# Performance work log

Hardware: AMD Instinct MI355X
Metric: run time of the kernel (lower is better)

Reference implementation:

```python
import jax, jax.numpy as jnp
import numpy as np

EPS = 1e-4  # matches normalize()/pixel_norm eps in the torch source
MP_T = 0.3  # mp_add mixing coefficient


def _weight_norm_1x1(w):
    # w: [out, in, 1, 1]; normalize each output filter (dims 1..3), alpha = 1/sqrt(fan_in),
    # then divide by sqrt(fan_in) as in Conv2d.forward (eval mode: no in-place copy).
    fan_in = w.shape[1] * w.shape[2] * w.shape[3]
    inv_sqrt_fan = np.float32(1.0 / np.sqrt(fan_in))
    n = jnp.sqrt(jnp.sum(w * w, axis=(1, 2, 3), keepdims=True))
    w_hat = w / (EPS + inv_sqrt_fan * n)
    return w_hat * inv_sqrt_fan


def _conv1x1(x, w):
    # 1x1 conv == channel GEMM
    return jnp.einsum('oc,bchw->bohw', _weight_norm_1x1(w)[:, :, 0, 0], x)


def _pixel_norm_last(x):
    # x / sqrt(mean(x^2, axis=-1) + eps)
    ms = jnp.mean(x * x, axis=-1, keepdims=True)
    return x * jax.lax.rsqrt(ms + EPS)


def setup_inputs() -> dict:
    key = jax.random.key(0)
    k1, k2, k3 = jax.random.split(key, 3)
    x = jax.random.normal(k1, (2, 256, 64, 64), dtype=jnp.float32)
    w_qkv = jax.random.normal(k2, (768, 256, 1, 1), dtype=jnp.float32)
    w_out = jax.random.normal(k3, (256, 256, 1, 1), dtype=jnp.float32)
    return {"x": x, "w_qkv": w_qkv, "w_out": w_out, "num_heads": 8}


def reference(x, w_qkv, w_out, num_heads):
    b, c, h, w = x.shape
    head_dim = c // num_heads
    qkv = _conv1x1(x, w_qkv)                      # [b, 3c, h, w]
    q, k, v = jnp.split(qkv, 3, axis=1)           # each [b, c, h, w]

    def to_heads(t):
        # [b, c, h, w] -> [b, heads, hw, head_dim]
        return t.reshape(b, num_heads, head_dim, h * w).transpose(0, 1, 3, 2)

    q = _pixel_norm_last(to_heads(q))
    k = _pixel_norm_last(to_heads(k))
    v = _pixel_norm_last(to_heads(v))

    scale = np.float32(1.0 / np.sqrt(head_dim))
    scores = jnp.einsum('bhqd,bhkd->bhqk', q, k) * scale
    attn = jax.nn.softmax(scores, axis=-1)
    y = jnp.einsum('bhqk,bhkd->bhqd', attn, v)    # [b, heads, hw, head_dim]
    y = y.transpose(0, 1, 3, 2).reshape(b, c, h, w)
    y = _conv1x1(y, w_out)

    # mp_add(x, y, t=0.3)
    t = np.float32(MP_T)
    inv_scale = np.float32(1.0 / np.sqrt(MP_T ** 2 + (1.0 - MP_T) ** 2))
    return ((1.0 - t) * x + t * y) * inv_scale
```

## Files before the change

kernel.cpp:

```cpp
#include <hip/hip_runtime.h>
#include <hip/hip_bf16.h>
#include <math.h>

#define S 4096
#define CIN 256
#define C3 768
#define NH 8
#define HD 32
#define KSPLIT 4

static constexpr float EPS = 1e-4f;

typedef __attribute__((ext_vector_type(8))) __bf16 bf16x8;
typedef __attribute__((ext_vector_type(4))) float f32x4;
typedef __attribute__((ext_vector_type(16))) float f32x16;
typedef __attribute__((ext_vector_type(4))) unsigned u32x4;

static inline __device__ ushort f2bf(float f) {
  unsigned u = __float_as_uint(f);
  return (ushort)((u + 0x7fffu + ((u >> 16) & 1u)) >> 16);
}
static inline __device__ float bf2f(ushort u) {
  return __uint_as_float((unsigned)u << 16);
}

static inline __device__ unsigned cvt_pk_bf16(float lo, float hi) {
  unsigned r;
  asm("v_cvt_pk_bf16_f32 %0, %1, %2" : "=v"(r) : "v"(lo), "v"(hi));
  return r;
}
static inline __device__ void plane32_swap(unsigned& a, unsigned& b) {
  asm("v_permlane32_swap_b32 %0, %1" : "+v"(a), "+v"(b));
}

#define EXP2 __builtin_amdgcn_exp2f


static inline __device__ void s_to_pf(const f32x16 s, bf16x8& plo, bf16x8& phi,
                                      float& lacc) {
  float e0 = EXP2(s[0]), e1 = EXP2(s[1]), e2 = EXP2(s[2]), e3 = EXP2(s[3]);
  float e4 = EXP2(s[4]), e5 = EXP2(s[5]), e6 = EXP2(s[6]), e7 = EXP2(s[7]);
  float e8 = EXP2(s[8]), e9 = EXP2(s[9]), e10 = EXP2(s[10]), e11 = EXP2(s[11]);
  float e12 = EXP2(s[12]), e13 = EXP2(s[13]), e14 = EXP2(s[14]), e15 = EXP2(s[15]);
  lacc += (((e0 + e1) + (e2 + e3)) + ((e4 + e5) + (e6 + e7))) +
          (((e8 + e9) + (e10 + e11)) + ((e12 + e13) + (e14 + e15)));
  unsigned c0 = cvt_pk_bf16(e0, e1);
  unsigned c1 = cvt_pk_bf16(e2, e3);
  unsigned c2 = cvt_pk_bf16(e4, e5);
  unsigned c3 = cvt_pk_bf16(e6, e7);
  plane32_swap(c0, c2);
  plane32_swap(c1, c3);
  u32x4 lo4 = {c0, c1, c2, c3};
  plo = __builtin_bit_cast(bf16x8, lo4);
  unsigned c4 = cvt_pk_bf16(e8, e9);
  unsigned c5 = cvt_pk_bf16(e10, e11);
  unsigned c6 = cvt_pk_bf16(e12, e13);
  unsigned c7 = cvt_pk_bf16(e14, e15);
  plane32_swap(c4, c6);
  plane32_swap(c5, c7);
  u32x4 hi4 = {c4, c5, c6, c7};
  phi = __builtin_bit_cast(bf16x8, hi4);
}

__global__ __launch_bounds__(256) void wnorm_kernel(const float* __restrict__ w_qkv,
                                                    const float* __restrict__ w_out,
                                                    ushort* __restrict__ wqb,
                                                    ushort* __restrict__ wob) {
  const int row = blockIdx.x * 4 + (threadIdx.x >> 6);
  const int lane = threadIdx.x & 63;
  const bool is_q = row < C3;
  const int r2 = is_q ? row : row - C3;
  const float* wr = (is_q ? w_qkv : w_out) + (size_t)r2 * CIN;
  float v[4];
  #pragma unroll
  for (int i = 0; i < 4; i++) v[i] = wr[lane + 64 * i];
  float ss = v[0] * v[0] + v[1] * v[1] + v[2] * v[2] + v[3] * v[3];
  #pragma unroll
  for (int off = 32; off > 0; off >>= 1) ss += __shfl_down(ss, off, 64);
  ss = __shfl(ss, 0, 64);
  const float scale = 1.0f / (sqrtf(ss) + 16.0f * EPS);
  ushort* whr = (is_q ? wqb : wob);
  #pragma unroll
  for (int i = 0; i < 4; i++) {
    const int c = lane + 64 * i;
    whr[((size_t)(r2 >> 4) * (CIN / 32) + (c >> 5)) * 512 + (r2 & 15) * 32 + (c & 31)] =
        f2bf(v[i] * scale);
  }
}

__global__ __launch_bounds__(256) void xt_kernel(const float* __restrict__ X,
                                                 ushort* __restrict__ Xt) {
  const int b = blockIdx.z;
  const int s0 = blockIdx.x * 64, c0 = blockIdx.y * 64;
  __shared__ ushort T[64][72];
  const int tc = threadIdx.x >> 4;
  const int ts = threadIdx.x & 15;
  #pragma unroll
  for (int i = 0; i < 4; i++) {
    const float4 v = *(const float4*)&X[((size_t)(b * CIN + c0 + tc + 16 * i)) * S + s0 + ts * 4];
    ushort4 u;
    u.x = f2bf(v.x); u.y = f2bf(v.y); u.z = f2bf(v.z); u.w = f2bf(v.w);
    *(ushort4*)&T[tc + 16 * i][ts * 4] = u;
  }
  __syncthreads();
  #pragma unroll
  for (int i = 0; i < 4; i++) {
    const int sr = tc + 16 * i;
    const int s = s0 + sr;
    const int c = c0 + ts * 4;
    ushort4 u;
    u.x = T[ts * 4 + 0][sr];
    u.y = T[ts * 4 + 1][sr];
    u.z = T[ts * 4 + 2][sr];
    u.w = T[ts * 4 + 3][sr];
    *(ushort4*)&Xt[(((size_t)b * (S / 16) + (s >> 4)) * (CIN / 32) + (c >> 5)) * 512 +
                   (s & 15) * 32 + (c & 31)] = u;
  }
}

__global__ __launch_bounds__(256) void conv1_fused_kernel(const ushort* __restrict__ W,
                                                          const ushort* __restrict__ Bm,
                                                          ushort* __restrict__ Qn,
                                                          ushort* __restrict__ Kn,
                                                          ushort* __restrict__ Vt) {
  const int b = blockIdx.z;
  const int wid = threadIdx.x >> 6, lane = threadIdx.x & 63;
  const int col = lane & 15, quad = lane >> 4;
  const int m0 = blockIdx.y * 64 + (wid >> 1) * 32;
  const int n0 = blockIdx.x * 128 + (wid & 1) * 64;
  const ushort* Bb = Bm + (size_t)b * (S / 16) * (CIN / 32) * 512;
  const int lofs = col * 32 + quad * 8;
  f32x4 acc[2][4] = {};
  #pragma unroll
  for (int k0 = 0; k0 < CIN; k0 += 32) {
    bf16x8 af[2], bf[4];
    #pragma unroll
    for (int mi = 0; mi < 2; mi++)
      af[mi] = *(const bf16x8*)&W[((size_t)(m0 / 16 + mi) * (CIN / 32) + (k0 >> 5)) * 512 + lofs];
    #pragma unroll
    for (int ni = 0; ni < 4; ni++)
      bf[ni] = *(const bf16x8*)&Bb[((size_t)(n0 / 16 + ni) * (CIN / 32) + (k0 >> 5)) * 512 + lofs];
    #pragma unroll
    for (int mi = 0; mi < 2; mi++)
      #pragma unroll
      for (int ni = 0; ni < 4; ni++)
        acc[mi][ni] = __builtin_amdgcn_mfma_f32_16x16x32_bf16(af[mi], bf[ni], acc[mi][ni], 0, 0, 0);
  }

  const int g = m0 >> 5;
  const int h = g & 7;
  float rn[4];
  #pragma unroll
  for (int ni = 0; ni < 4; ni++) {
    float ss = 0.f;
    #pragma unroll
    for (int mi = 0; mi < 2; mi++)
      #pragma unroll
      for (int r = 0; r < 4; r++) ss += acc[mi][ni][r] * acc[mi][ni][r];
    ss += __shfl_xor(ss, 16, 64);
    ss += __shfl_xor(ss, 32, 64);
    rn[ni] = rsqrtf(ss * (1.0f / HD) + EPS);
    if (g < 8) rn[ni] *= 0.2550348190698169f;
  }

  if (g < 8) {
    ushort* dst = Qn + (size_t)(b * NH + h) * S * HD;
    #pragma unroll
    for (int mi = 0; mi < 2; mi++)
      #pragma unroll
      for (int ni = 0; ni < 4; ni++) {
        ushort4 u;
        u.x = f2bf(acc[mi][ni][0] * rn[ni]);
        u.y = f2bf(acc[mi][ni][1] * rn[ni]);
        u.z = f2bf(acc[mi][ni][2] * rn[ni]);
        u.w = f2bf(acc[mi][ni][3] * rn[ni]);
        *(ushort4*)&dst[(size_t)(n0 + ni * 16 + col) * HD + mi * 16 + quad * 4] = u;
      }
  } else if (g < 16) {
    ushort* dst = Kn + (size_t)(b * NH + h) * S * HD + (size_t)(n0 >> 5) * 1024;
    #pragma unroll
    for (int mi = 0; mi < 2; mi++)
      #pragma unroll
      for (int ni = 0; ni < 4; ni++) {
        ushort4 u;
        u.x = f2bf(acc[mi][ni][0] * rn[ni]);
        u.y = f2bf(acc[mi][ni][1] * rn[ni]);
        u.z = f2bf(acc[mi][ni][2] * rn[ni]);
        u.w = f2bf(acc[mi][ni][3] * rn[ni]);
        *(ushort4*)&dst[(ni >> 1) * 1024 + mi * 512 + ((ni & 1) * 16 + col) * 16 +
                        (quad >> 1) * 8 + (quad & 1) * 4] = u;
      }
  } else {
    ushort* dst = Vt + (size_t)(b * NH + h) * HD * S + (size_t)(n0 >> 6) * 2048;
    #pragma unroll
    for (int mi = 0; mi < 2; mi++)
      #pragma unroll
      for (int ni = 0; ni < 4; ni++)
        #pragma unroll
        for (int r = 0; r < 4; r++)
          dst[ni * 512 + (mi * 16 + quad * 4 + r) * 16 + col] =
              f2bf(acc[mi][ni][r] * rn[ni]);
  }
}

__global__ __launch_bounds__(256, 4) void attn_kernel(const ushort* __restrict__ Qn,
                                                      const ushort* __restrict__ Kn,
                                                      const ushort* __restrict__ Vt,
                                                      ushort* __restrict__ accPb,
                                                      float* __restrict__ lP) {
  const int NWG = (S / 256) * NH * KSPLIT * 2;
  const int bid = blockIdx.x;
  const int id = (bid & 7) * (NWG / 8) + (bid >> 3);
  const int qt = id & 15;
  const int grp = id >> 4;
  const int h = grp & 7;
  const int kp = (grp >> 3) & (KSPLIT - 1);
  const int b = (grp >> 3) / KSPLIT;
  const int wid = threadIdx.x >> 6, lane = threadIdx.x & 63;
  const int ln = lane & 31, hi = lane >> 5;
  const int qA = qt * 256 + wid * 64;
  const int qB = qA + 32;

  const ushort* Qh = Qn + (size_t)(b * NH + h) * S * HD;

  bf16x8 qfA0 = *(const bf16x8*)&Qh[(size_t)(qA + ln) * HD + hi * 8];
  bf16x8 qfA1 = *(const bf16x8*)&Qh[(size_t)(qA + ln) * HD + 16 + hi * 8];
  bf16x8 qfB0 = *(const bf16x8*)&Qh[(size_t)(qB + ln) * HD + hi * 8];
  bf16x8 qfB1 = *(const bf16x8*)&Qh[(size_t)(qB + ln) * HD + 16 + hi * 8];

  const f32x16 z = {};
  f32x16 accA = {}, accB = {};
  float laccA = 0.f, laccB = 0.f;

  const int kt0 = kp * (S / KSPLIT);
  const int loff = (ln * 2 + hi) * 8;
  const ushort* Kp = Kn + (size_t)(b * NH + h) * S * HD + (size_t)kt0 * 32 + loff;
  const ushort* Vp = Vt + (size_t)(b * NH + h) * HD * S + (size_t)kt0 * 32 + loff;

  bf16x8 kf0 = *(const bf16x8*)&Kp[0];
  bf16x8 kf1 = *(const bf16x8*)&Kp[512];
  bf16x8 vf0 = *(const bf16x8*)&Vp[0];
  bf16x8 vf1 = *(const bf16x8*)&Vp[512];

  #pragma unroll 1
  for (int it = 0; it < S / KSPLIT / 32; ++it) {
    f32x16 sA = __builtin_amdgcn_mfma_f32_32x32x16_bf16(kf0, qfA0, z, 0, 0, 0);
    sA = __builtin_amdgcn_mfma_f32_32x32x16_bf16(kf1, qfA1, sA, 0, 0, 0);
    f32x16 sB = __builtin_amdgcn_mfma_f32_32x32x16_bf16(kf0, qfB0, z, 0, 0, 0);
    sB = __builtin_amdgcn_mfma_f32_32x32x16_bf16(kf1, qfB1, sB, 0, 0, 0);
    Kp += 1024;
    kf0 = *(const bf16x8*)&Kp[0];
    kf1 = *(const bf16x8*)&Kp[512];

    bf16x8 pfA0, pfA1;
    s_to_pf(sA, pfA0, pfA1, laccA);
    accA = __builtin_amdgcn_mfma_f32_32x32x16_bf16(vf0, pfA0, accA, 0, 0, 0);
    accA = __builtin_amdgcn_mfma_f32_32x32x16_bf16(vf1, pfA1, accA, 0, 0, 0);

    bf16x8 pfB0, pfB1;
    s_to_pf(sB, pfB0, pfB1, laccB);
    accB = __builtin_amdgcn_mfma_f32_32x32x16_bf16(vf0, pfB0, accB, 0, 0, 0);
    accB = __builtin_amdgcn_mfma_f32_32x32x16_bf16(vf1, pfB1, accB, 0, 0, 0);

    Vp += 1024;
    vf0 = *(const bf16x8*)&Vp[0];
    vf1 = *(const bf16x8*)&Vp[512];
  }

  ushort* ap = accPb + ((size_t)((kp * 2 + b) * NH + h)) * S * HD;
  const size_t rowA = (size_t)(qA + ln) * HD;
  const size_t rowB = (size_t)(qB + ln) * HD;
  #pragma unroll
  for (int g = 0; g < 4; g++) {
    uint2 u;
    u.x = cvt_pk_bf16(accA[4 * g + 0], accA[4 * g + 1]);
    u.y = cvt_pk_bf16(accA[4 * g + 2], accA[4 * g + 3]);
    *(uint2*)&ap[rowA + g * 8 + hi * 4] = u;
    uint2 v;
    v.x = cvt_pk_bf16(accB[4 * g + 0], accB[4 * g + 1]);
    v.y = cvt_pk_bf16(accB[4 * g + 2], accB[4 * g + 3]);
    *(uint2*)&ap[rowB + g * 8 + hi * 4] = v;
  }
  const float lsA = laccA + __shfl_xor(laccA, 32, 64);
  const float lsB = laccB + __shfl_xor(laccB, 32, 64);
  if (hi == 0) {
    float* lp = lP + ((size_t)((kp * 2 + b) * NH + h)) * S;
    lp[qA + ln] = lsA;
    lp[qB + ln] = lsB;
  }
}

__global__ __launch_bounds__(256) void combine_kernel(const ushort* __restrict__ accPb,
                                                      const float* __restrict__ lP,
                                                      ushort* __restrict__ Yt) {
  const int tid = blockIdx.x * 256 + threadIdx.x;
  const int dg = tid & 7;
  const int q = (tid >> 3) & (S - 1);
  const int h = (tid >> 15) & 7;
  const int b = tid >> 18;
  const size_t i0 = ((size_t)(b * NH + h)) * S + q;
  const size_t part = (size_t)2 * NH * S;
  float sx = 0.f, sy = 0.f, sz = 0.f, sw = 0.f, L = 0.f;
  #pragma unroll
  for (int p = 0; p < KSPLIT; p++) {
    const ushort4 a = *(const ushort4*)&accPb[(size_t)p * part * HD + i0 * HD + dg * 4];
    sx += bf2f(a.x); sy += bf2f(a.y); sz += bf2f(a.z); sw += bf2f(a.w);
    L += lP[(size_t)p * part + i0];
  }
  const float rl = 1.0f / L;
  ushort4 o;
  o.x = f2bf(sx * rl);
  o.y = f2bf(sy * rl);
  o.z = f2bf(sz * rl);
  o.w = f2bf(sw * rl);
  *(ushort4*)&Yt[(((size_t)b * (S / 16) + (q >> 4)) * (CIN / 32) + h) * 512 +
                 (q & 15) * 32 + dg * 4] = o;
}

__global__ __launch_bounds__(256) void conv2_kernel(const ushort* __restrict__ W,
                                                    const ushort* __restrict__ Bm,
                                                    const float* __restrict__ RES,
                                                    float* __restrict__ OUT) {
  const int b = blockIdx.z;
  const int wid = threadIdx.x >> 6, lane = threadIdx.x & 63;
  const int col = lane & 15, quad = lane >> 4;
  const int m0 = blockIdx.y * 64 + (wid >> 1) * 32;
  const int n0 = blockIdx.x * 64 + (wid & 1) * 32;
  const ushort* Bb = Bm + (size_t)b * (S / 16) * (CIN / 32) * 512;
  const int lofs = col * 32 + quad * 8;
  f32x4 acc[2][2] = {};
  #pragma unroll
  for (int k0 = 0; k0 < CIN; k0 += 32) {
    bf16x8 af[2], bf[2];
    #pragma unroll
    for (int mi = 0; mi < 2; mi++)
      af[mi] = *(const bf16x8*)&W[((size_t)(m0 / 16 + mi) * (CIN / 32) + (k0 >> 5)) * 512 + lofs];
    #pragma unroll
    for (int ni = 0; ni < 2; ni++)
      bf[ni] = *(const bf16x8*)&Bb[((size_t)(n0 / 16 + ni) * (CIN / 32) + (k0 >> 5)) * 512 + lofs];
    #pragma unroll
    for (int mi = 0; mi < 2; mi++)
      #pragma unroll
      for (int ni = 0; ni < 2; ni++)
        acc[mi][ni] = __builtin_amdgcn_mfma_f32_16x16x32_bf16(af[mi], bf[ni], acc[mi][ni], 0, 0, 0);
  }
  const float tc = 0.3f, om = 0.7f, inv = 1.3130643285972254f;
  #pragma unroll
  for (int mi = 0; mi < 2; mi++)
    #pragma unroll
    for (int ni = 0; ni < 2; ni++)
      #pragma unroll
      for (int r = 0; r < 4; r++) {
        const size_t idx = ((size_t)(b * CIN + m0 + mi * 16 + quad * 4 + r)) * S + n0 + ni * 16 + col;
        OUT[idx] = (om * RES[idx] + tc * acc[mi][ni][r]) * inv;
      }
}

extern "C" void kernel_launch(void* const* d_in, const int* in_sizes, int n_in,
                              void* d_out, int out_size, void* d_ws, size_t ws_size,
                              hipStream_t stream) {
  const float* x = (const float*)d_in[0];
  const float* w_qkv = (const float*)d_in[1];
  const float* w_out = (const float*)d_in[2];
  float* out = (float*)d_out;

  ushort* p = (ushort*)d_ws;
  ushort* wqb = p; p += (size_t)C3 * CIN;
  ushort* wob = p; p += (size_t)CIN * CIN;
  ushort* Qn = p; p += (size_t)2 * NH * S * HD;
  ushort* Kn = p; p += (size_t)2 * NH * S * HD;
  ushort* Vt = p; p += (size_t)2 * NH * S * HD;
  ushort* Yt = p; p += (size_t)2 * S * CIN;
  ushort* R = p; p += (size_t)KSPLIT * 2 * NH * S * HD;
  ushort* Xt = R;
  ushort* accPb = R;
  float* lP = (float*)p;

  wnorm_kernel<<<(C3 + CIN) / 4, 256, 0, stream>>>(w_qkv, w_out, wqb, wob);
  xt_kernel<<<dim3(S / 64, CIN / 64, 2), 256, 0, stream>>>(x, Xt);
  conv1_fused_kernel<<<dim3(S / 128, C3 / 64, 2), 256, 0, stream>>>(wqb, Xt, Qn, Kn, Vt);
  attn_kernel<<<(S / 256) * NH * KSPLIT * 2, 256, 0, stream>>>(Qn, Kn, Vt, accPb, lP);
  combine_kernel<<<2048, 256, 0, stream>>>(accPb, lP, Yt);
  conv2_kernel<<<dim3(S / 64, CIN / 64, 2), 256, 0, stream>>>(wob, Yt, x, out);
}
```

Before: 144.6 us.

## Compute softmax row sums via MFMA with ones and shrink conv1 N tile

The attention loop no longer sums the exponentials with VALU adds. It issues extra MFMAs that multiply the bf16 probabilities by a ones matrix, so the row sums come out of the matrix cores. This shifts work off the VALU, which is busy with exp2 and conversions, at the cost of doubling the PV-stage MFMA count, two extra 16-float accumulators per wave, and row sums taken from bf16-rounded probabilities. Separately, the conv1 kernel's per-wave N tile shrinks from 64 to 32 columns, doubling the grid to raise occupancy, with the K and V store indexing adjusted to match.

```diff
diff --git a/kernel.cpp b/kernel.cpp
--- a/kernel.cpp
+++ b/kernel.cpp
@@ -14,6 +14,7 @@
 typedef __attribute__((ext_vector_type(8))) __bf16 bf16x8;
 typedef __attribute__((ext_vector_type(4))) float f32x4;
 typedef __attribute__((ext_vector_type(16))) float f32x16;
+typedef __attribute__((ext_vector_type(8))) unsigned short u16x8;
 typedef __attribute__((ext_vector_type(4))) unsigned u32x4;
 
 static inline __device__ ushort f2bf(float f) {
@@ -36,26 +37,19 @@
 #define EXP2 __builtin_amdgcn_exp2f
 
 
-static inline __device__ void s_to_pf(const f32x16 s, bf16x8& plo, bf16x8& phi,
-                                      float& lacc) {
-  float e0 = EXP2(s[0]), e1 = EXP2(s[1]), e2 = EXP2(s[2]), e3 = EXP2(s[3]);
-  float e4 = EXP2(s[4]), e5 = EXP2(s[5]), e6 = EXP2(s[6]), e7 = EXP2(s[7]);
-  float e8 = EXP2(s[8]), e9 = EXP2(s[9]), e10 = EXP2(s[10]), e11 = EXP2(s[11]);
-  float e12 = EXP2(s[12]), e13 = EXP2(s[13]), e14 = EXP2(s[14]), e15 = EXP2(s[15]);
-  lacc += (((e0 + e1) + (e2 + e3)) + ((e4 + e5) + (e6 + e7))) +
-          (((e8 + e9) + (e10 + e11)) + ((e12 + e13) + (e14 + e15)));
-  unsigned c0 = cvt_pk_bf16(e0, e1);
-  unsigned c1 = cvt_pk_bf16(e2, e3);
-  unsigned c2 = cvt_pk_bf16(e4, e5);
-  unsigned c3 = cvt_pk_bf16(e6, e7);
+static inline __device__ void s_to_pf(const f32x16 s, bf16x8& plo, bf16x8& phi) {
+  unsigned c0 = cvt_pk_bf16(EXP2(s[0]), EXP2(s[1]));
+  unsigned c1 = cvt_pk_bf16(EXP2(s[2]), EXP2(s[3]));
+  unsigned c2 = cvt_pk_bf16(EXP2(s[4]), EXP2(s[5]));
+  unsigned c3 = cvt_pk_bf16(EXP2(s[6]), EXP2(s[7]));
   plane32_swap(c0, c2);
   plane32_swap(c1, c3);
   u32x4 lo4 = {c0, c1, c2, c3};
   plo = __builtin_bit_cast(bf16x8, lo4);
-  unsigned c4 = cvt_pk_bf16(e8, e9);
-  unsigned c5 = cvt_pk_bf16(e10, e11);
-  unsigned c6 = cvt_pk_bf16(e12, e13);
-  unsigned c7 = cvt_pk_bf16(e14, e15);
+  unsigned c4 = cvt_pk_bf16(EXP2(s[8]), EXP2(s[9]));
+  unsigned c5 = cvt_pk_bf16(EXP2(s[10]), EXP2(s[11]));
+  unsigned c6 = cvt_pk_bf16(EXP2(s[12]), EXP2(s[13]));
+  unsigned c7 = cvt_pk_bf16(EXP2(s[14]), EXP2(s[15]));
   plane32_swap(c4, c6);
   plane32_swap(c5, c7);
   u32x4 hi4 = {c4, c5, c6, c7};
@@ -127,31 +121,31 @@
   const int wid = threadIdx.x >> 6, lane = threadIdx.x & 63;
   const int col = lane & 15, quad = lane >> 4;
   const int m0 = blockIdx.y * 64 + (wid >> 1) * 32;
-  const int n0 = blockIdx.x * 128 + (wid & 1) * 64;
+  const int n0 = blockIdx.x * 64 + (wid & 1) * 32;
   const ushort* Bb = Bm + (size_t)b * (S / 16) * (CIN / 32) * 512;
   const int lofs = col * 32 + quad * 8;
-  f32x4 acc[2][4] = {};
+  f32x4 acc[2][2] = {};
   #pragma unroll
   for (int k0 = 0; k0 < CIN; k0 += 32) {
-    bf16x8 af[2], bf[4];
+    bf16x8 af[2], bf[2];
     #pragma unroll
     for (int mi = 0; mi < 2; mi++)
       af[mi] = *(const bf16x8*)&W[((size_t)(m0 / 16 + mi) * (CIN / 32) + (k0 >> 5)) * 512 + lofs];
     #pragma unroll
-    for (int ni = 0; ni < 4; ni++)
+    for (int ni = 0; ni < 2; ni++)
       bf[ni] = *(const bf16x8*)&Bb[((size_t)(n0 / 16 + ni) * (CIN / 32) + (k0 >> 5)) * 512 + lofs];
     #pragma unroll
     for (int mi = 0; mi < 2; mi++)
       #pragma unroll
-      for (int ni = 0; ni < 4; ni++)
+      for (int ni = 0; ni < 2; ni++)
         acc[mi][ni] = __builtin_amdgcn_mfma_f32_16x16x32_bf16(af[mi], bf[ni], acc[mi][ni], 0, 0, 0);
   }
 
   const int g = m0 >> 5;
   const int h = g & 7;
-  float rn[4];
-  #pragma unroll
-  for (int ni = 0; ni < 4; ni++) {
+  float rn[2];
+  #pragma unroll
+  for (int ni = 0; ni < 2; ni++) {
     float ss = 0.f;
     #pragma unroll
     for (int mi = 0; mi < 2; mi++)
@@ -168,7 +162,7 @@
     #pragma unroll
     for (int mi = 0; mi < 2; mi++)
       #pragma unroll
-      for (int ni = 0; ni < 4; ni++) {
+      for (int ni = 0; ni < 2; ni++) {
         ushort4 u;
         u.x = f2bf(acc[mi][ni][0] * rn[ni]);
         u.y = f2bf(acc[mi][ni][1] * rn[ni]);
@@ -181,24 +175,25 @@
     #pragma unroll
     for (int mi = 0; mi < 2; mi++)
       #pragma unroll
-      for (int ni = 0; ni < 4; ni++) {
+      for (int ni = 0; ni < 2; ni++) {
         ushort4 u;
         u.x = f2bf(acc[mi][ni][0] * rn[ni]);
         u.y = f2bf(acc[mi][ni][1] * rn[ni]);
         u.z = f2bf(acc[mi][ni][2] * rn[ni]);
         u.w = f2bf(acc[mi][ni][3] * rn[ni]);
-        *(ushort4*)&dst[(ni >> 1) * 1024 + mi * 512 + ((ni & 1) * 16 + col) * 16 +
+        *(ushort4*)&dst[mi * 512 + (ni * 16 + col) * 16 +
                         (quad >> 1) * 8 + (quad & 1) * 4] = u;
       }
   } else {
     ushort* dst = Vt + (size_t)(b * NH + h) * HD * S + (size_t)(n0 >> 6) * 2048;
-    #pragma unroll
-    for (int mi = 0; mi < 2; mi++)
-      #pragma unroll
-      for (int ni = 0; ni < 4; ni++)
+    const int kcbase = (n0 & 32) >> 4;
+    #pragma unroll
+    for (int mi = 0; mi < 2; mi++)
+      #pragma unroll
+      for (int ni = 0; ni < 2; ni++)
         #pragma unroll
         for (int r = 0; r < 4; r++)
-          dst[ni * 512 + (mi * 16 + quad * 4 + r) * 16 + col] =
+          dst[(kcbase + ni) * 512 + (mi * 16 + quad * 4 + r) * 16 + col] =
               f2bf(acc[mi][ni][r] * rn[ni]);
   }
 }
@@ -228,9 +223,11 @@
   bf16x8 qfB0 = *(const bf16x8*)&Qh[(size_t)(qB + ln) * HD + hi * 8];
   bf16x8 qfB1 = *(const bf16x8*)&Qh[(size_t)(qB + ln) * HD + 16 + hi * 8];
 
+  const u16x8 ou = {0x3F80, 0x3F80, 0x3F80, 0x3F80, 0x3F80, 0x3F80, 0x3F80, 0x3F80};
+  const bf16x8 ones = __builtin_bit_cast(bf16x8, ou);
   const f32x16 z = {};
   f32x16 accA = {}, accB = {};
-  float laccA = 0.f, laccB = 0.f;
+  f32x16 acclA = {}, acclB = {};
 
   const int kt0 = kp * (S / KSPLIT);
   const int loff = (ln * 2 + hi) * 8;
@@ -253,14 +250,18 @@
     kf1 = *(const bf16x8*)&Kp[512];
 
     bf16x8 pfA0, pfA1;
-    s_to_pf(sA, pfA0, pfA1, laccA);
+    s_to_pf(sA, pfA0, pfA1);
     accA = __builtin_amdgcn_mfma_f32_32x32x16_bf16(vf0, pfA0, accA, 0, 0, 0);
+    acclA = __builtin_amdgcn_mfma_f32_32x32x16_bf16(ones, pfA0, acclA, 0, 0, 0);
     accA = __builtin_amdgcn_mfma_f32_32x32x16_bf16(vf1, pfA1, accA, 0, 0, 0);
+    acclA = __builtin_amdgcn_mfma_f32_32x32x16_bf16(ones, pfA1, acclA, 0, 0, 0);
 
     bf16x8 pfB0, pfB1;
-    s_to_pf(sB, pfB0, pfB1, laccB);
+    s_to_pf(sB, pfB0, pfB1);
     accB = __builtin_amdgcn_mfma_f32_32x32x16_bf16(vf0, pfB0, accB, 0, 0, 0);
+    acclB = __builtin_amdgcn_mfma_f32_32x32x16_bf16(ones, pfB0, acclB, 0, 0, 0);
     accB = __builtin_amdgcn_mfma_f32_32x32x16_bf16(vf1, pfB1, accB, 0, 0, 0);
+    acclB = __builtin_amdgcn_mfma_f32_32x32x16_bf16(ones, pfB1, acclB, 0, 0, 0);
 
     Vp += 1024;
     vf0 = *(const bf16x8*)&Vp[0];
@@ -281,12 +282,10 @@
     v.y = cvt_pk_bf16(accB[4 * g + 2], accB[4 * g + 3]);
     *(uint2*)&ap[rowB + g * 8 + hi * 4] = v;
   }
-  const float lsA = laccA + __shfl_xor(laccA, 32, 64);
-  const float lsB = laccB + __shfl_xor(laccB, 32, 64);
   if (hi == 0) {
     float* lp = lP + ((size_t)((kp * 2 + b) * NH + h)) * S;
-    lp[qA + ln] = lsA;
-    lp[qB + ln] = lsB;
+    lp[qA + ln] = acclA[0];
+    lp[qB + ln] = acclB[0];
   }
 }
 
@@ -378,7 +377,7 @@
 
   wnorm_kernel<<<(C3 + CIN) / 4, 256, 0, stream>>>(w_qkv, w_out, wqb, wob);
   xt_kernel<<<dim3(S / 64, CIN / 64, 2), 256, 0, stream>>>(x, Xt);
-  conv1_fused_kernel<<<dim3(S / 128, C3 / 64, 2), 256, 0, stream>>>(wqb, Xt, Qn, Kn, Vt);
+  conv1_fused_kernel<<<dim3(S / 64, C3 / 64, 2), 256, 0, stream>>>(wqb, Xt, Qn, Kn, Vt);
   attn_kernel<<<(S / 256) * NH * KSPLIT * 2, 256, 0, stream>>>(Qn, Kn, Vt, accPb, lP);
   combine_kernel<<<2048, 256, 0, stream>>>(accPb, lP, Yt);
   conv2_kernel<<<dim3(S / 64, CIN / 64, 2), 256, 0, stream>>>(wob, Yt, x, out);
```

Result: slower. 151.4 us (+4.7%).
